# Kernel optimization log

Hardware: AMD Instinct MI355X
Metric: run time of the kernel (lower is better)

The kernel has to match this reference:

```python
import jax, jax.numpy as jnp
import numpy as np

N, E, K = 50000, 800000, 16
D, H = 128, 8
DH = D // H
SCALE = D ** (-0.5)
EPS = 1e-5


def _ln(x, g, b):
    m = jnp.mean(x, axis=-1, keepdims=True)
    v = jnp.mean((x - m) ** 2, axis=-1, keepdims=True)
    return (x - m) * jax.lax.rsqrt(v + EPS) * g + b


def setup_inputs() -> dict:
    key = jax.random.key(0)
    ks = jax.random.split(key, 20)
    s = 0.02
    inp = {
        "triplet_h": jax.random.normal(ks[0], (N, D), jnp.float32),
        "mask_nodes": jnp.ones((N,), jnp.bool_),
        "src": jax.random.randint(ks[1], (E,), 0, N),
        "dst": jax.random.randint(ks[2], (E,), 0, N),
        "edge_bias": jax.random.normal(ks[3], (E, H), jnp.float32),
        "mask_edges": jnp.ones((E,), jnp.bool_),
        "inc_idx": jax.random.randint(ks[4], (N, K), 0, E),
        "inc_mask": jnp.ones((N, K), jnp.bool_),
        # params
        "ln1_g": jnp.ones((D,), jnp.float32),
        "ln1_b": jnp.zeros((D,), jnp.float32),
        "qkv_w": jax.random.normal(ks[5], (D, 3 * D), jnp.float32) * s,
        "qkv_b": jnp.zeros((3 * D,), jnp.float32),
        "res_in_w": jax.random.normal(ks[6], (D, D), jnp.float32) * s,
        "res_in_b": jnp.zeros((D,), jnp.float32),
        "res_ln_g": jnp.ones((D,), jnp.float32),
        "res_ln_b": jnp.zeros((D,), jnp.float32),
        "ffn_in_w": jax.random.normal(ks[7], (D, 4 * D), jnp.float32) * s,
        "ffn_in_b": jnp.zeros((4 * D,), jnp.float32),
        "ffn_out_w": jax.random.normal(ks[8], (4 * D, D), jnp.float32) * s,
        "ffn_out_b": jnp.zeros((D,), jnp.float32),
    }
    return inp


def reference(triplet_h, mask_nodes, src, dst, edge_bias, mask_edges, inc_idx,
              inc_mask, ln1_g, ln1_b, qkv_w, qkv_b, res_in_w, res_in_b,
              res_ln_g, res_ln_b, ffn_in_w, ffn_in_b, ffn_out_w, ffn_out_b):
    x = _ln(triplet_h, ln1_g, ln1_b)
    qkv = (x @ qkv_w + qkv_b).reshape(-1, 3, H, DH)
    q = qkv[:, 0] * SCALE  # [N,H,dh]
    k = qkv[:, 1]
    v = qkv[:, 2]

    zero_i = jnp.zeros_like(src)
    se = jnp.where(mask_edges, src, zero_i)
    de = jnp.where(mask_edges, dst, zero_i)

    dot_all = jnp.sum(q[se] * k[de], axis=-1)  # [E,H]
    me = mask_edges[:, None]
    dot_all = jnp.where(me, dot_all, 0.0)
    eb = jnp.where(me, edge_bias, 0.0)
    scores_all = dot_all + eb  # [E,H]

    v_src = jnp.where(me[:, :, None], v[se], 0.0)  # [E,H,dh]

    idx = jnp.clip(inc_idx, 0)  # [N,K]
    s_in = scores_all[idx]  # [N,K,H]
    v_in = v_src[idx]       # [N,K,H,dh]
    m_in = inc_mask & mask_nodes[:, None]
    s_in = jnp.where(m_in[:, :, None], s_in, -1e9)
    a_in = jax.nn.softmax(s_in, axis=1)  # [N,K,H]
    out = jnp.sum(v_in * a_in[..., None], axis=1).reshape(-1, H * DH)  # [N,D]

    # Residual block (dropout p=0)
    x2 = triplet_h + (out @ res_in_w + res_in_b)
    y = _ln(x2, res_ln_g, res_ln_b)
    y = jax.nn.gelu(y @ ffn_in_w + ffn_in_b) @ ffn_out_w + ffn_out_b
    return x2 + y
```

## Files before the change

### kernel.cpp

```cpp
#include <hip/hip_runtime.h>
#include <math.h>

#define N_NODES 50000
#define N_EDGES 800000
#define QSCALE 0.08838834764831845f
#define LEPS 1e-5f
#define S4 0.17f
#define INV_S4 (1.0f / S4)
#define SC4 (S4 * S4 * QSCALE)

typedef unsigned short ushort_t;
typedef unsigned char uchar_t;
typedef short bf16x8 __attribute__((ext_vector_type(8)));
typedef float f32x4 __attribute__((ext_vector_type(4)));
typedef float f32x2 __attribute__((ext_vector_type(2)));

__device__ __forceinline__ ushort_t f2b(float f) {
    unsigned int u = __float_as_uint(f);
    u += 0x7FFF + ((u >> 16) & 1);
    return (ushort_t)(u >> 16);
}
__device__ __forceinline__ float b2f(ushort_t v) {
    return __uint_as_float(((unsigned int)v) << 16);
}
__device__ __forceinline__ uchar_t f2fp8(float f) {
    unsigned int pk = __builtin_amdgcn_cvt_pk_fp8_f32(f, f, 0, false);
    return (uchar_t)(pk & 0xff);
}
__device__ __forceinline__ float gelu_f(float x) {
    float u = 1.5957691216057308f * (x + 0.044715f * x * x * x);
    float e = __expf(u);
    float t = 1.f - 2.f / (e + 1.f);
    return 0.5f * x * (1.f + t);
}
__device__ __forceinline__ void gload16(const ushort_t* g, ushort_t* l) {
    __builtin_amdgcn_global_load_lds(
        (const __attribute__((address_space(1))) unsigned int*)g,
        (__attribute__((address_space(3))) unsigned int*)l, 16, 0, 0);
}
__device__ __forceinline__ int frag_idx(int n7, int k7) {
    return ((n7 >> 4) * 4 + (k7 >> 5)) * 512 + ((k7 >> 3) & 3) * 128 + (n7 & 15) * 8 + (k7 & 7);
}
__device__ __forceinline__ int fidx64(int n7, int k6) {
    return ((n7 >> 4) * 2 + (k6 >> 5)) * 512 + ((k6 >> 3) & 3) * 128 + (n7 & 15) * 8 + (k6 & 7);
}

#if __has_builtin(__builtin_amdgcn_sdot8)
__device__ __forceinline__ int snib_dot(unsigned int a, unsigned int b, int acc) {
    return __builtin_amdgcn_sdot8((int)a, (int)b, acc, false);
}
#else
__device__ __forceinline__ int snib_dot(unsigned int a, unsigned int b, int acc) {
    #pragma unroll
    for (int i = 0; i < 8; ++i) {
        int av = (int)((a >> (4 * i)) & 15u); av = (av ^ 8) - 8;
        int bv = (int)((b >> (4 * i)) & 15u); bv = (bv ^ 8) - 8;
        acc += av * bv;
    }
    return acc;
}
#endif

__global__ __launch_bounds__(256) void k_prep(
    const float* __restrict__ qkvw, const float* __restrict__ riw,
    const float* __restrict__ fiw,  const float* __restrict__ fow,
    const int* __restrict__ src, const int* __restrict__ dst,
    const float* __restrict__ eb,
    ushort_t* __restrict__ qkvwT, ushort_t* __restrict__ riwT,
    ushort_t* __restrict__ fiwT,  ushort_t* __restrict__ fowT,
    uint4* __restrict__ edt)
{
    if (blockIdx.x >= 768) {
        int i = (blockIdx.x - 768) * 256 + threadIdx.x;
        if (i >= N_EDGES) return;
        float4 a = *(const float4*)(eb + (size_t)i * 8);
        float4 b = *(const float4*)(eb + (size_t)i * 8 + 4);
        uint4 r0, r1;
        r0.x = (unsigned int)src[i];
        r0.y = (unsigned int)dst[i];
        r0.z = (unsigned int)f2b(a.x) | ((unsigned int)f2b(a.y) << 16);
        r0.w = (unsigned int)f2b(a.z) | ((unsigned int)f2b(a.w) << 16);
        r1.x = (unsigned int)f2b(b.x) | ((unsigned int)f2b(b.y) << 16);
        r1.y = (unsigned int)f2b(b.z) | ((unsigned int)f2b(b.w) << 16);
        r1.z = 0; r1.w = 0;
        edt[(size_t)i * 2]     = r0;
        edt[(size_t)i * 2 + 1] = r1;
        return;
    }
    int i = blockIdx.x * 256 + threadIdx.x;
    if (i < 384 * 128) {
        int k = i / 384, n = i - k * 384;
        int ch = n >> 7, n7 = n & 127, half = k >> 6, k6 = k & 63;
        qkvwT[(size_t)(ch * 2 + half) * 8192 + fidx64(n7, k6)] = f2b(qkvw[i]);
        return;
    }
    i -= 384 * 128;
    if (i < 128 * 128) {
        int k = i >> 7, n = i & 127;
        riwT[frag_idx(n, k)] = f2b(riw[i]);
        return;
    }
    i -= 128 * 128;
    if (i < 512 * 128) {
        int k = i >> 9, n = i & 511;
        fiwT[(size_t)(n >> 7) * 16384 + frag_idx(n & 127, k)] = f2b(fiw[i]);
        return;
    }
    i -= 512 * 128;
    if (i < 128 * 512) {
        int k = i >> 7, n = i & 127;
        fowT[(size_t)(k >> 6) * 8192 + fidx64(n, k & 63)] = f2b(fow[i]);
    }
}

__global__ __launch_bounds__(256) void k1_ln_qkv(
    const float* __restrict__ th, const float* __restrict__ g1, const float* __restrict__ b1,
    const ushort_t* __restrict__ wT, const float* __restrict__ bias,
    uchar_t* __restrict__ q4, uchar_t* __restrict__ k4, uchar_t* __restrict__ v8)
{
    __shared__ __align__(16) ushort_t xs[64][136];
    __shared__ __align__(16) ushort_t wbuf[2][8192];
    const int tid = threadIdx.x, lane = tid & 63, w = tid >> 6;
    const int g0 = blockIdx.x * 64;
    uchar_t* sbuf8 = (uchar_t*)xs;

    #pragma unroll
    for (int t = 0; t < 4; ++t)
        gload16(wT + (size_t)(t * 256 + tid) * 8, wbuf[0] + (t * 256 + tid) * 8);

    float ga = g1[lane], gb = g1[lane + 64];
    float ba = b1[lane], bb = b1[lane + 64];
    for (int rr = 0; rr < 16; ++rr) {
        int r = w * 16 + rr, grow = g0 + r;
        float x0 = 0.f, x1 = 0.f;
        if (grow < N_NODES) {
            x0 = th[(size_t)grow * 128 + lane];
            x1 = th[(size_t)grow * 128 + 64 + lane];
        }
        float s1 = x0 + x1, s2 = x0 * x0 + x1 * x1;
        #pragma unroll
        for (int off = 32; off; off >>= 1) { s1 += __shfl_xor(s1, off); s2 += __shfl_xor(s2, off); }
        float m = s1 * (1.f / 128.f);
        float v = s2 * (1.f / 128.f) - m * m;
        float rs = rsqrtf(v + LEPS);
        xs[r][lane]      = f2b((x0 - m) * rs * ga + ba);
        xs[r][lane + 64] = f2b((x1 - m) * rs * gb + bb);
    }
    __syncthreads();

    const int q = lane >> 4, ml = lane & 15;
    const int rloc = w * 16 + q * 4;
    bf16x8 a[4];
    #pragma unroll
    for (int kc = 0; kc < 4; ++kc)
        a[kc] = *(const bf16x8*)&xs[w * 16 + ml][kc * 32 + q * 8];

    for (int ch = 0; ch < 3; ++ch) {
        f32x4 acc[8];
        #pragma unroll
        for (int t2 = 0; t2 < 8; ++t2) acc[t2] = (f32x4){0.f, 0.f, 0.f, 0.f};

        #pragma unroll
        for (int t = 0; t < 4; ++t)
            gload16(wT + (size_t)(ch * 2 + 1) * 8192 + (size_t)(t * 256 + tid) * 8,
                    wbuf[1] + (t * 256 + tid) * 8);
        {
            const bf16x8* wb8 = (const bf16x8*)wbuf[0];
            #pragma unroll
            for (int t2 = 0; t2 < 8; ++t2)
                #pragma unroll
                for (int kc2 = 0; kc2 < 2; ++kc2)
                    acc[t2] = __builtin_amdgcn_mfma_f32_16x16x32_bf16(
                        a[kc2], wb8[(t2 * 2 + kc2) * 64 + lane], acc[t2], 0, 0, 0);
        }
        __syncthreads();

        if (ch < 2) {
            #pragma unroll
            for (int t = 0; t < 4; ++t)
                gload16(wT + (size_t)(ch + 1) * 2 * 8192 + (size_t)(t * 256 + tid) * 8,
                        wbuf[0] + (t * 256 + tid) * 8);
        }
        {
            const bf16x8* wb8 = (const bf16x8*)wbuf[1];
            #pragma unroll
            for (int t2 = 0; t2 < 8; ++t2)
                #pragma unroll
                for (int kc2 = 0; kc2 < 2; ++kc2)
                    acc[t2] = __builtin_amdgcn_mfma_f32_16x16x32_bf16(
                        a[2 + kc2], wb8[(t2 * 2 + kc2) * 64 + lane], acc[t2], 0, 0, 0);
        }
        __syncthreads();

        #pragma unroll
        for (int t2 = 0; t2 < 8; ++t2) {
            int n = t2 * 16 + ml;
            float bs = bias[ch * 128 + n];
            #pragma unroll
            for (int r = 0; r < 4; ++r) {
                float val = acc[t2][r] + bs;
                if (ch < 2) {
                    float enc = rintf(val * INV_S4) + 8.f;
                    enc = fminf(fmaxf(enc, 0.f), 15.f);
                    sbuf8[(rloc + r) * 128 + n] = ((uchar_t)enc) ^ 8;
                } else {
                    sbuf8[(rloc + r) * 128 + n] = f2fp8(val);
                }
            }
        }
        __syncthreads();
        if (ch < 2) {
            uchar_t* outp = (ch == 0) ? q4 : k4;
            int grow = g0 + (tid >> 2);
            if (grow < N_NODES) {
                const uchar_t* in = sbuf8 + (tid >> 2) * 128 + (tid & 3) * 32;
                uint4 o;
                unsigned int* ow = (unsigned int*)&o;
                #pragma unroll
                for (int wd = 0; wd < 4; ++wd) {
                    unsigned int x = 0;
                    #pragma unroll
                    for (int b = 0; b < 4; ++b) {
                        unsigned int lo = in[wd * 8 + 2 * b];
                        unsigned int hi = in[wd * 8 + 2 * b + 1];
                        x |= (lo | (hi << 4)) << (8 * b);
                    }
                    ow[wd] = x;
                }
                *(uint4*)(outp + (size_t)grow * 64 + (tid & 3) * 16) = o;
            }
        } else {
            int grow = g0 + (tid >> 2);
            if (grow < N_NODES) {
                uint4 v0 = *(const uint4*)(sbuf8 + tid * 32);
                uint4 v1 = *(const uint4*)(sbuf8 + tid * 32 + 16);
                *(uint4*)(v8 + (size_t)grow * 128 + (tid & 3) * 32) = v0;
                *(uint4*)(v8 + (size_t)grow * 128 + (tid & 3) * 32 + 16) = v1;
            }
        }
    }
}

__global__ __launch_bounds__(256) void k23_agg(
    const uchar_t* __restrict__ q4, const uchar_t* __restrict__ k4,
    const uchar_t* __restrict__ v8,
    const uint4* __restrict__ edt,
    const int* __restrict__ inc_idx,
    ushort_t* __restrict__ outw)
{
    __shared__ int ss[256];
    __shared__ float sc[16 * 144];
    const int tid = threadIdx.x;
    const int nb = blockIdx.x * 16;

    {
        int e = inc_idx[(size_t)nb * 16 + tid];
        if (e < 0) e = 0;
        uint4 r0 = edt[(size_t)e * 2];
        uint4 r1 = edt[(size_t)e * 2 + 1];
        int s = (int)r0.x, d = (int)r0.y;
        ss[tid] = s;
        const uint4 qa = *(const uint4*)(q4 + (size_t)s * 64);
        const uint4 qb = *(const uint4*)(q4 + (size_t)s * 64 + 16);
        const uint4 qc = *(const uint4*)(q4 + (size_t)s * 64 + 32);
        const uint4 qd = *(const uint4*)(q4 + (size_t)s * 64 + 48);
        const uint4 ka = *(const uint4*)(k4 + (size_t)d * 64);
        const uint4 kb = *(const uint4*)(k4 + (size_t)d * 64 + 16);
        const uint4 kc = *(const uint4*)(k4 + (size_t)d * 64 + 32);
        const uint4 kd = *(const uint4*)(k4 + (size_t)d * 64 + 48);
        int d0 = snib_dot(qa.x, ka.x, snib_dot(qa.y, ka.y, 0));
        int d1 = snib_dot(qa.z, ka.z, snib_dot(qa.w, ka.w, 0));
        int d2 = snib_dot(qb.x, kb.x, snib_dot(qb.y, kb.y, 0));
        int d3 = snib_dot(qb.z, kb.z, snib_dot(qb.w, kb.w, 0));
        int d4 = snib_dot(qc.x, kc.x, snib_dot(qc.y, kc.y, 0));
        int d5 = snib_dot(qc.z, kc.z, snib_dot(qc.w, kc.w, 0));
        int d6 = snib_dot(qd.x, kd.x, snib_dot(qd.y, kd.y, 0));
        int d7 = snib_dot(qd.z, kd.z, snib_dot(qd.w, kd.w, 0));
        float* scn = sc + (tid >> 4) * 144 + (tid & 15) * 9;
        scn[0] = (float)d0 * SC4 + b2f((ushort_t)(r0.z & 0xffff));
        scn[1] = (float)d1 * SC4 + b2f((ushort_t)(r0.z >> 16));
        scn[2] = (float)d2 * SC4 + b2f((ushort_t)(r0.w & 0xffff));
        scn[3] = (float)d3 * SC4 + b2f((ushort_t)(r0.w >> 16));
        scn[4] = (float)d4 * SC4 + b2f((ushort_t)(r1.x & 0xffff));
        scn[5] = (float)d5 * SC4 + b2f((ushort_t)(r1.x >> 16));
        scn[6] = (float)d6 * SC4 + b2f((ushort_t)(r1.y & 0xffff));
        scn[7] = (float)d7 * SC4 + b2f((ushort_t)(r1.y >> 16));
    }
    __syncthreads();

    const int node = tid >> 4;
    const int lx = tid & 15;
    const int h = lx >> 1;
    const int j0 = lx * 8;
    const float* scn = sc + node * 144 + h;
    float m = -1e30f;
    #pragma unroll
    for (int k = 0; k < 16; k++) m = fmaxf(m, scn[k * 9]);
    float p[16];
    float sum = 0.f;
    #pragma unroll
    for (int k = 0; k < 16; k++) { p[k] = __expf(scn[k * 9] - m); sum += p[k]; }
    float inv = 1.f / sum;
    f32x2 A0 = {0.f, 0.f}, A1 = {0.f, 0.f}, A2 = {0.f, 0.f}, A3 = {0.f, 0.f};
    #pragma unroll
    for (int k = 0; k < 16; k++) {
        int sn = ss[node * 16 + k];
        uint2 vv = *(const uint2*)(v8 + (size_t)sn * 128 + j0);
        f32x2 u0 = __builtin_amdgcn_cvt_pk_f32_fp8(vv.x, false);
        f32x2 u1 = __builtin_amdgcn_cvt_pk_f32_fp8(vv.x, true);
        f32x2 u2 = __builtin_amdgcn_cvt_pk_f32_fp8(vv.y, false);
        f32x2 u3 = __builtin_amdgcn_cvt_pk_f32_fp8(vv.y, true);
        f32x2 pk2 = {p[k], p[k]};
        A0 += u0 * pk2; A1 += u1 * pk2; A2 += u2 * pk2; A3 += u3 * pk2;
    }
    uint4 o;
    o.x = (unsigned int)f2b(A0.x * inv) | ((unsigned int)f2b(A0.y * inv) << 16);
    o.y = (unsigned int)f2b(A1.x * inv) | ((unsigned int)f2b(A1.y * inv) << 16);
    o.z = (unsigned int)f2b(A2.x * inv) | ((unsigned int)f2b(A2.y * inv) << 16);
    o.w = (unsigned int)f2b(A3.x * inv) | ((unsigned int)f2b(A3.y * inv) << 16);
    *(uint4*)(outw + (size_t)(nb + node) * 128 + j0) = o;
}

__global__ __launch_bounds__(256) void k4_ffn(
    const float* __restrict__ th, const ushort_t* __restrict__ outw,
    const ushort_t* __restrict__ riwT, const float* __restrict__ rib,
    const float* __restrict__ rlg, const float* __restrict__ rlb,
    const ushort_t* __restrict__ fiwT, const float* __restrict__ fib,
    const ushort_t* __restrict__ fowT, const float* __restrict__ fob,
    float* __restrict__ dout)
{
    __shared__ __align__(16) ushort_t sbuf[64][136];
    __shared__ __align__(16) ushort_t wbuf[2][8192];
    const int tid = threadIdx.x, lane = tid & 63, w = tid >> 6;
    const int g0 = blockIdx.x * 64;
    const int q = lane >> 4, ml = lane & 15;
    const int rloc = w * 16 + q * 4;
    const int aswz = (ml >> 2) & 3;
    const bf16x8* wb0 = (const bf16x8*)wbuf[0];
    const bf16x8* wb1 = (const bf16x8*)wbuf[1];

    #pragma unroll
    for (int t = 0; t < 4; ++t)
        gload16(riwT + (size_t)(t * 256 + tid) * 8, wbuf[0] + (t * 256 + tid) * 8);
    int arow = g0 + w * 16 + ml; if (arow > N_NODES - 1) arow = N_NODES - 1;
    bf16x8 a[4];
    #pragma unroll
    for (int kc = 0; kc < 4; ++kc)
        a[kc] = *(const bf16x8*)(outw + (size_t)arow * 128 + kc * 32 + q * 8);
    float tv[8][4];
    #pragma unroll
    for (int t = 0; t < 8; ++t)
        #pragma unroll
        for (int r = 0; r < 4; ++r) {
            int grow = g0 + rloc + r;
            tv[t][r] = (grow < N_NODES) ? th[(size_t)grow * 128 + t * 16 + ml] : 0.f;
        }
    __syncthreads();

    f32x4 acc[8];

    #pragma unroll
    for (int t = 0; t < 4; ++t)
        gload16(riwT + 8192 + (size_t)(t * 256 + tid) * 8, wbuf[1] + (t * 256 + tid) * 8);
    #pragma unroll
    for (int t2 = 0; t2 < 4; ++t2) {
        f32x4 z = {0.f, 0.f, 0.f, 0.f};
        #pragma unroll
        for (int kc = 0; kc < 4; ++kc)
            z = __builtin_amdgcn_mfma_f32_16x16x32_bf16(
                a[kc], wb0[(t2 * 4 + kc) * 64 + lane], z, 0, 0, 0);
        acc[t2] = z;
    }
    __syncthreads();

    #pragma unroll
    for (int t = 0; t < 4; ++t)
        gload16(fiwT + (size_t)(t * 256 + tid) * 8, wbuf[0] + (t * 256 + tid) * 8);
    #pragma unroll
    for (int t2 = 0; t2 < 4; ++t2) {
        f32x4 z = {0.f, 0.f, 0.f, 0.f};
        #pragma unroll
        for (int kc = 0; kc < 4; ++kc)
            z = __builtin_amdgcn_mfma_f32_16x16x32_bf16(
                a[kc], wb1[(t2 * 4 + kc) * 64 + lane], z, 0, 0, 0);
        acc[4 + t2] = z;
    }
    #pragma unroll
    for (int t = 0; t < 8; ++t) {
        float bb = rib[t * 16 + ml];
        #pragma unroll
        for (int r = 0; r < 4; ++r)
            acc[t][r] += bb + tv[t][r];
    }
    {
        float rg[8], rbv[8];
        #pragma unroll
        for (int t = 0; t < 8; ++t) { rg[t] = rlg[t * 16 + ml]; rbv[t] = rlb[t * 16 + ml]; }
        #pragma unroll
        for (int r = 0; r < 4; ++r) {
            float s1 = 0.f, s2 = 0.f;
            #pragma unroll
            for (int t = 0; t < 8; ++t) { float v = acc[t][r]; s1 += v; s2 += v * v; }
            #pragma unroll
            for (int off = 1; off < 16; off <<= 1) { s1 += __shfl_xor(s1, off); s2 += __shfl_xor(s2, off); }
            float m = s1 * (1.f / 128.f);
            float v = s2 * (1.f / 128.f) - m * m;
            float rs = rsqrtf(v + LEPS);
            #pragma unroll
            for (int t = 0; t < 8; ++t) {
                int G = (2 * t + (ml >> 3)) ^ q;
                sbuf[rloc + r][G * 8 + (ml & 7)] = f2b((acc[t][r] - m) * rs * rg[t] + rbv[t]);
            }
        }
    }
    bf16x8 a2[4];
    #pragma unroll
    for (int kc = 0; kc < 4; ++kc)
        a2[kc] = *(const bf16x8*)&sbuf[w * 16 + ml][(((kc * 4 + q) ^ aswz) << 3)];
    __syncthreads();

    for (int f = 0; f < 8; ++f) {
        #pragma unroll
        for (int t = 0; t < 4; ++t)
            gload16(fowT + (size_t)f * 8192 + (size_t)(t * 256 + tid) * 8,
                    wbuf[1] + (t * 256 + tid) * 8);
        #pragma unroll
        for (int t2 = 0; t2 < 4; ++t2) {
            f32x4 hacc = {0.f, 0.f, 0.f, 0.f};
            #pragma unroll
            for (int kc = 0; kc < 4; ++kc)
                hacc = __builtin_amdgcn_mfma_f32_16x16x32_bf16(
                    a2[kc], wb0[(t2 * 4 + kc) * 64 + lane], hacc, 0, 0, 0);
            float fb = fib[f * 64 + t2 * 16 + ml];
            int G = (2 * t2 + (ml >> 3)) ^ q;
            #pragma unroll
            for (int r = 0; r < 4; ++r)
                sbuf[rloc + r][G * 8 + (ml & 7)] = f2b(gelu_f(hacc[r] + fb));
        }
        bf16x8 a3[2];
        #pragma unroll
        for (int kc2 = 0; kc2 < 2; ++kc2)
            a3[kc2] = *(const bf16x8*)&sbuf[w * 16 + ml][(((kc2 * 4 + q) ^ aswz) << 3)];
        __syncthreads();

        if (f < 7) {
            #pragma unroll
            for (int t = 0; t < 4; ++t)
                gload16(fiwT + (size_t)(f + 1) * 8192 + (size_t)(t * 256 + tid) * 8,
                        wbuf[0] + (t * 256 + tid) * 8);
        }
        #pragma unroll
        for (int t = 0; t < 8; ++t) {
            #pragma unroll
            for (int kc2 = 0; kc2 < 2; ++kc2)
                acc[t] = __builtin_amdgcn_mfma_f32_16x16x32_bf16(
                    a3[kc2], wb1[(t * 2 + kc2) * 64 + lane], acc[t], 0, 0, 0);
        }
        __syncthreads();
    }

    #pragma unroll
    for (int t = 0; t < 8; ++t) {
        float ob = fob[t * 16 + ml];
        #pragma unroll
        for (int r = 0; r < 4; ++r) {
            int grow = g0 + rloc + r;
            if (grow < N_NODES)
                dout[(size_t)grow * 128 + t * 16 + ml] = acc[t][r] + ob;
        }
    }
}

extern "C" void kernel_launch(void* const* d_in, const int* in_sizes, int n_in,
                              void* d_out, int out_size, void* d_ws, size_t ws_size,
                              hipStream_t stream)
{
    const float* th    = (const float*)d_in[0];
    const int*   src   = (const int*)d_in[2];
    const int*   dst   = (const int*)d_in[3];
    const float* ebias = (const float*)d_in[4];
    const int*   inc   = (const int*)d_in[6];
    const float* ln1g  = (const float*)d_in[8];
    const float* ln1b  = (const float*)d_in[9];
    const float* qkvw  = (const float*)d_in[10];
    const float* qkvb  = (const float*)d_in[11];
    const float* riw   = (const float*)d_in[12];
    const float* rib   = (const float*)d_in[13];
    const float* rlg   = (const float*)d_in[14];
    const float* rlb   = (const float*)d_in[15];
    const float* fiw   = (const float*)d_in[16];
    const float* fib   = (const float*)d_in[17];
    const float* fow   = (const float*)d_in[18];
    const float* fob   = (const float*)d_in[19];

    char* ws = (char*)d_ws;
    uchar_t* q4      = (uchar_t*)ws;                               ws += (size_t)N_NODES * 64;
    uchar_t* k4t     = (uchar_t*)ws;                               ws += (size_t)N_NODES * 64;
    uchar_t* v8      = (uchar_t*)ws;                               ws += (size_t)N_NODES * 128;
    ushort_t* outw   = (ushort_t*)ws;                              ws += (size_t)N_NODES * 128 * 2;
    ushort_t* qkvwT  = (ushort_t*)ws;                              ws += (size_t)384 * 128 * 2;
    ushort_t* riwT   = (ushort_t*)ws;                              ws += (size_t)128 * 128 * 2;
    ushort_t* fiwT   = (ushort_t*)ws;                              ws += (size_t)512 * 128 * 2;
    ushort_t* fowT   = (ushort_t*)ws;                              ws += (size_t)128 * 512 * 2;
    uint4*    edt    = (uint4*)ws;                                 ws += (size_t)N_EDGES * 32;
    float* dout = (float*)d_out;

    k_prep<<<768 + (N_EDGES + 255) / 256, 256, 0, stream>>>(
        qkvw, riw, fiw, fow, src, dst, ebias, qkvwT, riwT, fiwT, fowT, edt);
    k1_ln_qkv<<<(N_NODES + 63) / 64, 256, 0, stream>>>(th, ln1g, ln1b, qkvwT, qkvb, q4, k4t, v8);
    k23_agg<<<N_NODES / 16, 256, 0, stream>>>(q4, k4t, v8, edt, inc, outw);
    k4_ffn<<<(N_NODES + 63) / 64, 256, 0, stream>>>(th, outw, riwT, rib, rlg, rlb,
                                                    fiwT, fib, fowT, fob, dout);
}
```

Measured before the change: 275.1 us.

## Split FFN kernel output columns across wave pairs with 512-thread blocks

The fused residual/LN/FFN kernel now runs 512 threads per block: each 16-row group is handled by two waves, each owning half of the 128 output columns. LayerNorm statistics are combined across the wave pair through a small shared-memory reduction. Biases and gamma/beta are preloaded into registers, and the weight-tile loads are rescheduled. The aim is to halve per-wave accumulator registers and MFMA work so more waves are resident and latency is better hidden. The cost is extra __syncthreads and more barrier stalls per FFN chunk.

```diff
diff --git a/kernel.cpp b/kernel.cpp
--- a/kernel.cpp
+++ b/kernel.cpp
@@ -321,7 +321,7 @@
     *(uint4*)(outw + (size_t)(nb + node) * 128 + j0) = o;
 }
 
-__global__ __launch_bounds__(256) void k4_ffn(
+__global__ __launch_bounds__(512, 4) void k4_ffn(
     const float* __restrict__ th, const ushort_t* __restrict__ outw,
     const ushort_t* __restrict__ riwT, const float* __restrict__ rib,
     const float* __restrict__ rlg, const float* __restrict__ rlb,
@@ -331,142 +331,150 @@
 {
     __shared__ __align__(16) ushort_t sbuf[64][136];
     __shared__ __align__(16) ushort_t wbuf[2][8192];
+    __shared__ float lnred[4][16][2][2];
     const int tid = threadIdx.x, lane = tid & 63, w = tid >> 6;
+    const int p = w >> 1, hn = w & 1;
     const int g0 = blockIdx.x * 64;
     const int q = lane >> 4, ml = lane & 15;
-    const int rloc = w * 16 + q * 4;
+    const int rloc = p * 16 + q * 4;
     const int aswz = (ml >> 2) & 3;
     const bf16x8* wb0 = (const bf16x8*)wbuf[0];
     const bf16x8* wb1 = (const bf16x8*)wbuf[1];
 
     #pragma unroll
-    for (int t = 0; t < 4; ++t)
-        gload16(riwT + (size_t)(t * 256 + tid) * 8, wbuf[0] + (t * 256 + tid) * 8);
-    int arow = g0 + w * 16 + ml; if (arow > N_NODES - 1) arow = N_NODES - 1;
+    for (int t = 0; t < 2; ++t)
+        gload16(riwT + (size_t)(t * 512 + tid) * 8, wbuf[0] + (t * 512 + tid) * 8);
+    #pragma unroll
+    for (int t = 0; t < 2; ++t)
+        gload16(riwT + 8192 + (size_t)(t * 512 + tid) * 8, wbuf[1] + (t * 512 + tid) * 8);
+
+    int arow = g0 + p * 16 + ml; if (arow > N_NODES - 1) arow = N_NODES - 1;
     bf16x8 a[4];
     #pragma unroll
     for (int kc = 0; kc < 4; ++kc)
         a[kc] = *(const bf16x8*)(outw + (size_t)arow * 128 + kc * 32 + q * 8);
-    float tv[8][4];
-    #pragma unroll
-    for (int t = 0; t < 8; ++t)
+    float tv[4][4];
+    #pragma unroll
+    for (int t = 0; t < 4; ++t)
         #pragma unroll
         for (int r = 0; r < 4; ++r) {
             int grow = g0 + rloc + r;
-            tv[t][r] = (grow < N_NODES) ? th[(size_t)grow * 128 + t * 16 + ml] : 0.f;
-        }
-    __syncthreads();
-
-    f32x4 acc[8];
-
-    #pragma unroll
-    for (int t = 0; t < 4; ++t)
-        gload16(riwT + 8192 + (size_t)(t * 256 + tid) * 8, wbuf[1] + (t * 256 + tid) * 8);
-    #pragma unroll
-    for (int t2 = 0; t2 < 4; ++t2) {
+            tv[t][r] = (grow < N_NODES) ? th[(size_t)grow * 128 + hn * 64 + t * 16 + ml] : 0.f;
+        }
+    float fibr[16];
+    #pragma unroll
+    for (int f = 0; f < 8; ++f)
+        #pragma unroll
+        for (int t2 = 0; t2 < 2; ++t2)
+            fibr[f * 2 + t2] = fib[f * 64 + (hn * 2 + t2) * 16 + ml];
+    float rbias[4], rg[4], rbv[4], fb4[4];
+    #pragma unroll
+    for (int t = 0; t < 4; ++t) {
+        int c = hn * 64 + t * 16 + ml;
+        rbias[t] = rib[c]; rg[t] = rlg[c]; rbv[t] = rlb[c]; fb4[t] = fob[c];
+    }
+    __syncthreads();
+
+    const bf16x8* wbg = hn ? wb1 : wb0;
+    f32x4 acc[4];
+    #pragma unroll
+    for (int t = 0; t < 4; ++t) {
         f32x4 z = {0.f, 0.f, 0.f, 0.f};
         #pragma unroll
         for (int kc = 0; kc < 4; ++kc)
             z = __builtin_amdgcn_mfma_f32_16x16x32_bf16(
-                a[kc], wb0[(t2 * 4 + kc) * 64 + lane], z, 0, 0, 0);
-        acc[t2] = z;
-    }
-    __syncthreads();
-
-    #pragma unroll
-    for (int t = 0; t < 4; ++t)
-        gload16(fiwT + (size_t)(t * 256 + tid) * 8, wbuf[0] + (t * 256 + tid) * 8);
-    #pragma unroll
-    for (int t2 = 0; t2 < 4; ++t2) {
-        f32x4 z = {0.f, 0.f, 0.f, 0.f};
-        #pragma unroll
-        for (int kc = 0; kc < 4; ++kc)
-            z = __builtin_amdgcn_mfma_f32_16x16x32_bf16(
-                a[kc], wb1[(t2 * 4 + kc) * 64 + lane], z, 0, 0, 0);
-        acc[4 + t2] = z;
-    }
-    #pragma unroll
-    for (int t = 0; t < 8; ++t) {
-        float bb = rib[t * 16 + ml];
-        #pragma unroll
-        for (int r = 0; r < 4; ++r)
-            acc[t][r] += bb + tv[t][r];
-    }
-    {
-        float rg[8], rbv[8];
-        #pragma unroll
-        for (int t = 0; t < 8; ++t) { rg[t] = rlg[t * 16 + ml]; rbv[t] = rlb[t * 16 + ml]; }
-        #pragma unroll
-        for (int r = 0; r < 4; ++r) {
-            float s1 = 0.f, s2 = 0.f;
-            #pragma unroll
-            for (int t = 0; t < 8; ++t) { float v = acc[t][r]; s1 += v; s2 += v * v; }
-            #pragma unroll
-            for (int off = 1; off < 16; off <<= 1) { s1 += __shfl_xor(s1, off); s2 += __shfl_xor(s2, off); }
-            float m = s1 * (1.f / 128.f);
-            float v = s2 * (1.f / 128.f) - m * m;
-            float rs = rsqrtf(v + LEPS);
-            #pragma unroll
-            for (int t = 0; t < 8; ++t) {
-                int G = (2 * t + (ml >> 3)) ^ q;
-                sbuf[rloc + r][G * 8 + (ml & 7)] = f2b((acc[t][r] - m) * rs * rg[t] + rbv[t]);
-            }
-        }
-    }
+                a[kc], wbg[(t * 4 + kc) * 64 + lane], z, 0, 0, 0);
+        #pragma unroll
+        for (int r = 0; r < 4; ++r) z[r] += rbias[t] + tv[t][r];
+        acc[t] = z;
+    }
+    float ps1[4], ps2[4];
+    #pragma unroll
+    for (int r = 0; r < 4; ++r) {
+        float s1 = 0.f, s2 = 0.f;
+        #pragma unroll
+        for (int t = 0; t < 4; ++t) { float v = acc[t][r]; s1 += v; s2 += v * v; }
+        #pragma unroll
+        for (int off = 1; off < 16; off <<= 1) { s1 += __shfl_xor(s1, off); s2 += __shfl_xor(s2, off); }
+        ps1[r] = s1; ps2[r] = s2;
+        if (ml == 0) { lnred[p][q * 4 + r][hn][0] = s1; lnred[p][q * 4 + r][hn][1] = s2; }
+    }
+    __syncthreads();
+    #pragma unroll
+    for (int r = 0; r < 4; ++r) {
+        float s1 = ps1[r] + lnred[p][q * 4 + r][hn ^ 1][0];
+        float s2 = ps2[r] + lnred[p][q * 4 + r][hn ^ 1][1];
+        float m = s1 * (1.f / 128.f);
+        float v = s2 * (1.f / 128.f) - m * m;
+        float rs = rsqrtf(v + LEPS);
+        #pragma unroll
+        for (int t = 0; t < 4; ++t) {
+            int G = (2 * (hn * 4 + t) + (ml >> 3)) ^ q;
+            sbuf[rloc + r][G * 8 + (ml & 7)] = f2b((acc[t][r] - m) * rs * rg[t] + rbv[t]);
+        }
+    }
+    __syncthreads();
     bf16x8 a2[4];
     #pragma unroll
     for (int kc = 0; kc < 4; ++kc)
-        a2[kc] = *(const bf16x8*)&sbuf[w * 16 + ml][(((kc * 4 + q) ^ aswz) << 3)];
+        a2[kc] = *(const bf16x8*)&sbuf[p * 16 + ml][(((kc * 4 + q) ^ aswz) << 3)];
+    __syncthreads();
+    #pragma unroll
+    for (int t = 0; t < 2; ++t)
+        gload16(fiwT + (size_t)(t * 512 + tid) * 8, wbuf[0] + (t * 512 + tid) * 8);
+    #pragma unroll
+    for (int t = 0; t < 2; ++t)
+        gload16(fowT + (size_t)(t * 512 + tid) * 8, wbuf[1] + (t * 512 + tid) * 8);
     __syncthreads();
 
     for (int f = 0; f < 8; ++f) {
         #pragma unroll
-        for (int t = 0; t < 4; ++t)
-            gload16(fowT + (size_t)f * 8192 + (size_t)(t * 256 + tid) * 8,
-                    wbuf[1] + (t * 256 + tid) * 8);
-        #pragma unroll
-        for (int t2 = 0; t2 < 4; ++t2) {
+        for (int t2 = 0; t2 < 2; ++t2) {
             f32x4 hacc = {0.f, 0.f, 0.f, 0.f};
             #pragma unroll
             for (int kc = 0; kc < 4; ++kc)
                 hacc = __builtin_amdgcn_mfma_f32_16x16x32_bf16(
-                    a2[kc], wb0[(t2 * 4 + kc) * 64 + lane], hacc, 0, 0, 0);
-            float fb = fib[f * 64 + t2 * 16 + ml];
-            int G = (2 * t2 + (ml >> 3)) ^ q;
+                    a2[kc], wb0[((hn * 2 + t2) * 4 + kc) * 64 + lane], hacc, 0, 0, 0);
+            float fb = fibr[f * 2 + t2];
+            int G = (2 * (hn * 2 + t2) + (ml >> 3)) ^ q;
             #pragma unroll
             for (int r = 0; r < 4; ++r)
                 sbuf[rloc + r][G * 8 + (ml & 7)] = f2b(gelu_f(hacc[r] + fb));
         }
+        __syncthreads();
+        if (f < 7) {
+            #pragma unroll
+            for (int t = 0; t < 2; ++t)
+                gload16(fiwT + (size_t)(f + 1) * 8192 + (size_t)(t * 512 + tid) * 8,
+                        wbuf[0] + (t * 512 + tid) * 8);
+        }
         bf16x8 a3[2];
         #pragma unroll
         for (int kc2 = 0; kc2 < 2; ++kc2)
-            a3[kc2] = *(const bf16x8*)&sbuf[w * 16 + ml][(((kc2 * 4 + q) ^ aswz) << 3)];
-        __syncthreads();
-
-        if (f < 7) {
-            #pragma unroll
-            for (int t = 0; t < 4; ++t)
-                gload16(fiwT + (size_t)(f + 1) * 8192 + (size_t)(t * 256 + tid) * 8,
-                        wbuf[0] + (t * 256 + tid) * 8);
-        }
-        #pragma unroll
-        for (int t = 0; t < 8; ++t) {
+            a3[kc2] = *(const bf16x8*)&sbuf[p * 16 + ml][(((kc2 * 4 + q) ^ aswz) << 3)];
+        #pragma unroll
+        for (int t = 0; t < 4; ++t) {
             #pragma unroll
             for (int kc2 = 0; kc2 < 2; ++kc2)
                 acc[t] = __builtin_amdgcn_mfma_f32_16x16x32_bf16(
-                    a3[kc2], wb1[(t * 2 + kc2) * 64 + lane], acc[t], 0, 0, 0);
+                    a3[kc2], wb1[((hn * 4 + t) * 2 + kc2) * 64 + lane], acc[t], 0, 0, 0);
         }
         __syncthreads();
-    }
-
-    #pragma unroll
-    for (int t = 0; t < 8; ++t) {
-        float ob = fob[t * 16 + ml];
+        if (f < 7) {
+            #pragma unroll
+            for (int t = 0; t < 2; ++t)
+                gload16(fowT + (size_t)(f + 1) * 8192 + (size_t)(t * 512 + tid) * 8,
+                        wbuf[1] + (t * 512 + tid) * 8);
+        }
+    }
+
+    #pragma unroll
+    for (int t = 0; t < 4; ++t) {
         #pragma unroll
         for (int r = 0; r < 4; ++r) {
             int grow = g0 + rloc + r;
             if (grow < N_NODES)
-                dout[(size_t)grow * 128 + t * 16 + ml] = acc[t][r] + ob;
+                dout[(size_t)grow * 128 + hn * 64 + t * 16 + ml] = acc[t][r] + fb4[t];
         }
     }
 }
@@ -509,6 +517,6 @@
         qkvw, riw, fiw, fow, src, dst, ebias, qkvwT, riwT, fiwT, fowT, edt);
     k1_ln_qkv<<<(N_NODES + 63) / 64, 256, 0, stream>>>(th, ln1g, ln1b, qkvwT, qkvb, q4, k4t, v8);
     k23_agg<<<N_NODES / 16, 256, 0, stream>>>(q4, k4t, v8, edt, inc, outw);
-    k4_ffn<<<(N_NODES + 63) / 64, 256, 0, stream>>>(th, outw, riwT, rib, rlg, rlb,
+    k4_ffn<<<(N_NODES + 63) / 64, 512, 0, stream>>>(th, outw, riwT, rib, rlg, rlb,
                                                     fiwT, fib, fowT, fob, dout);
 }
```

Result: no change. 270.3 us (-1.7%).

## Double FFN kernel row tile to 128 rows per block to reuse staged weights

Applied to the files above, without the earlier changes.

The fused residual/FFN kernel now processes 128 node rows per 256-thread block, with each wave handling two 16-row MMA tiles. Every weight chunk staged in shared memory is therefore used for twice as many rows, which halves global weight traffic and the per-row cost of barriers. The residual input load moves after the first GEMM to ease register pressure, and a minimum of two blocks per CU is requested. The trade-off is twice the accumulator registers, a larger shared buffer, and half as many blocks, which can lower occupancy or cause spills.

```diff
diff --git a/kernel.cpp b/kernel.cpp
--- a/kernel.cpp
+++ b/kernel.cpp
@@ -321,7 +321,7 @@
     *(uint4*)(outw + (size_t)(nb + node) * 128 + j0) = o;
 }
 
-__global__ __launch_bounds__(256) void k4_ffn(
+__global__ __launch_bounds__(256, 2) void k4_ffn(
     const float* __restrict__ th, const ushort_t* __restrict__ outw,
     const ushort_t* __restrict__ riwT, const float* __restrict__ rib,
     const float* __restrict__ rlg, const float* __restrict__ rlb,
@@ -329,12 +329,11 @@
     const ushort_t* __restrict__ fowT, const float* __restrict__ fob,
     float* __restrict__ dout)
 {
-    __shared__ __align__(16) ushort_t sbuf[64][136];
+    __shared__ __align__(16) ushort_t sbuf[128][136];
     __shared__ __align__(16) ushort_t wbuf[2][8192];
     const int tid = threadIdx.x, lane = tid & 63, w = tid >> 6;
-    const int g0 = blockIdx.x * 64;
+    const int g0 = blockIdx.x * 128;
     const int q = lane >> 4, ml = lane & 15;
-    const int rloc = w * 16 + q * 4;
     const int aswz = (ml >> 2) & 3;
     const bf16x8* wb0 = (const bf16x8*)wbuf[0];
     const bf16x8* wb1 = (const bf16x8*)wbuf[1];
@@ -342,81 +341,94 @@
     #pragma unroll
     for (int t = 0; t < 4; ++t)
         gload16(riwT + (size_t)(t * 256 + tid) * 8, wbuf[0] + (t * 256 + tid) * 8);
-    int arow = g0 + w * 16 + ml; if (arow > N_NODES - 1) arow = N_NODES - 1;
-    bf16x8 a[4];
-    #pragma unroll
-    for (int kc = 0; kc < 4; ++kc)
-        a[kc] = *(const bf16x8*)(outw + (size_t)arow * 128 + kc * 32 + q * 8);
-    float tv[8][4];
-    #pragma unroll
-    for (int t = 0; t < 8; ++t)
-        #pragma unroll
-        for (int r = 0; r < 4; ++r) {
-            int grow = g0 + rloc + r;
-            tv[t][r] = (grow < N_NODES) ? th[(size_t)grow * 128 + t * 16 + ml] : 0.f;
-        }
+    bf16x8 a[2][4];
+    #pragma unroll
+    for (int m2 = 0; m2 < 2; ++m2) {
+        int arow = g0 + w * 32 + m2 * 16 + ml;
+        if (arow > N_NODES - 1) arow = N_NODES - 1;
+        #pragma unroll
+        for (int kc = 0; kc < 4; ++kc)
+            a[m2][kc] = *(const bf16x8*)(outw + (size_t)arow * 128 + kc * 32 + q * 8);
+    }
     __syncthreads();
 
-    f32x4 acc[8];
+    f32x4 acc[2][8];
 
     #pragma unroll
     for (int t = 0; t < 4; ++t)
         gload16(riwT + 8192 + (size_t)(t * 256 + tid) * 8, wbuf[1] + (t * 256 + tid) * 8);
     #pragma unroll
-    for (int t2 = 0; t2 < 4; ++t2) {
-        f32x4 z = {0.f, 0.f, 0.f, 0.f};
-        #pragma unroll
-        for (int kc = 0; kc < 4; ++kc)
-            z = __builtin_amdgcn_mfma_f32_16x16x32_bf16(
-                a[kc], wb0[(t2 * 4 + kc) * 64 + lane], z, 0, 0, 0);
-        acc[t2] = z;
-    }
+    for (int m2 = 0; m2 < 2; ++m2)
+        #pragma unroll
+        for (int t2 = 0; t2 < 4; ++t2) {
+            f32x4 z = {0.f, 0.f, 0.f, 0.f};
+            #pragma unroll
+            for (int kc = 0; kc < 4; ++kc)
+                z = __builtin_amdgcn_mfma_f32_16x16x32_bf16(
+                    a[m2][kc], wb0[(t2 * 4 + kc) * 64 + lane], z, 0, 0, 0);
+            acc[m2][t2] = z;
+        }
     __syncthreads();
 
     #pragma unroll
     for (int t = 0; t < 4; ++t)
         gload16(fiwT + (size_t)(t * 256 + tid) * 8, wbuf[0] + (t * 256 + tid) * 8);
     #pragma unroll
-    for (int t2 = 0; t2 < 4; ++t2) {
-        f32x4 z = {0.f, 0.f, 0.f, 0.f};
-        #pragma unroll
-        for (int kc = 0; kc < 4; ++kc)
-            z = __builtin_amdgcn_mfma_f32_16x16x32_bf16(
-                a[kc], wb1[(t2 * 4 + kc) * 64 + lane], z, 0, 0, 0);
-        acc[4 + t2] = z;
-    }
-    #pragma unroll
-    for (int t = 0; t < 8; ++t) {
-        float bb = rib[t * 16 + ml];
-        #pragma unroll
-        for (int r = 0; r < 4; ++r)
-            acc[t][r] += bb + tv[t][r];
+    for (int m2 = 0; m2 < 2; ++m2)
+        #pragma unroll
+        for (int t2 = 0; t2 < 4; ++t2) {
+            f32x4 z = {0.f, 0.f, 0.f, 0.f};
+            #pragma unroll
+            for (int kc = 0; kc < 4; ++kc)
+                z = __builtin_amdgcn_mfma_f32_16x16x32_bf16(
+                    a[m2][kc], wb1[(t2 * 4 + kc) * 64 + lane], z, 0, 0, 0);
+            acc[m2][4 + t2] = z;
+        }
+    #pragma unroll
+    for (int m2 = 0; m2 < 2; ++m2) {
+        const int rloc = w * 32 + m2 * 16 + q * 4;
+        #pragma unroll
+        for (int t = 0; t < 8; ++t) {
+            float bb = rib[t * 16 + ml];
+            #pragma unroll
+            for (int r = 0; r < 4; ++r) {
+                int grow = g0 + rloc + r;
+                float tv = (grow < N_NODES) ? th[(size_t)grow * 128 + t * 16 + ml] : 0.f;
+                acc[m2][t][r] += bb + tv;
+            }
+        }
     }
     {
         float rg[8], rbv[8];
         #pragma unroll
         for (int t = 0; t < 8; ++t) { rg[t] = rlg[t * 16 + ml]; rbv[t] = rlb[t * 16 + ml]; }
         #pragma unroll
-        for (int r = 0; r < 4; ++r) {
-            float s1 = 0.f, s2 = 0.f;
-            #pragma unroll
-            for (int t = 0; t < 8; ++t) { float v = acc[t][r]; s1 += v; s2 += v * v; }
-            #pragma unroll
-            for (int off = 1; off < 16; off <<= 1) { s1 += __shfl_xor(s1, off); s2 += __shfl_xor(s2, off); }
-            float m = s1 * (1.f / 128.f);
-            float v = s2 * (1.f / 128.f) - m * m;
-            float rs = rsqrtf(v + LEPS);
-            #pragma unroll
-            for (int t = 0; t < 8; ++t) {
-                int G = (2 * t + (ml >> 3)) ^ q;
-                sbuf[rloc + r][G * 8 + (ml & 7)] = f2b((acc[t][r] - m) * rs * rg[t] + rbv[t]);
-            }
-        }
-    }
-    bf16x8 a2[4];
-    #pragma unroll
-    for (int kc = 0; kc < 4; ++kc)
-        a2[kc] = *(const bf16x8*)&sbuf[w * 16 + ml][(((kc * 4 + q) ^ aswz) << 3)];
+        for (int m2 = 0; m2 < 2; ++m2) {
+            const int rloc = w * 32 + m2 * 16 + q * 4;
+            #pragma unroll
+            for (int r = 0; r < 4; ++r) {
+                float s1 = 0.f, s2 = 0.f;
+                #pragma unroll
+                for (int t = 0; t < 8; ++t) { float v = acc[m2][t][r]; s1 += v; s2 += v * v; }
+                #pragma unroll
+                for (int off = 1; off < 16; off <<= 1) { s1 += __shfl_xor(s1, off); s2 += __shfl_xor(s2, off); }
+                float m = s1 * (1.f / 128.f);
+                float v = s2 * (1.f / 128.f) - m * m;
+                float rs = rsqrtf(v + LEPS);
+                #pragma unroll
+                for (int t = 0; t < 8; ++t) {
+                    int G = (2 * t + (ml >> 3)) ^ q;
+                    sbuf[rloc + r][G * 8 + (ml & 7)] = f2b((acc[m2][t][r] - m) * rs * rg[t] + rbv[t]);
+                }
+            }
+        }
+    }
+    bf16x8 a2[2][4];
+    #pragma unroll
+    for (int m2 = 0; m2 < 2; ++m2)
+        #pragma unroll
+        for (int kc = 0; kc < 4; ++kc)
+            a2[m2][kc] = *(const bf16x8*)&sbuf[w * 32 + m2 * 16 + ml][(((kc * 4 + q) ^ aswz) << 3)];
     __syncthreads();
 
     for (int f = 0; f < 8; ++f) {
@@ -425,22 +437,28 @@
             gload16(fowT + (size_t)f * 8192 + (size_t)(t * 256 + tid) * 8,
                     wbuf[1] + (t * 256 + tid) * 8);
         #pragma unroll
-        for (int t2 = 0; t2 < 4; ++t2) {
-            f32x4 hacc = {0.f, 0.f, 0.f, 0.f};
-            #pragma unroll
-            for (int kc = 0; kc < 4; ++kc)
-                hacc = __builtin_amdgcn_mfma_f32_16x16x32_bf16(
-                    a2[kc], wb0[(t2 * 4 + kc) * 64 + lane], hacc, 0, 0, 0);
-            float fb = fib[f * 64 + t2 * 16 + ml];
-            int G = (2 * t2 + (ml >> 3)) ^ q;
-            #pragma unroll
-            for (int r = 0; r < 4; ++r)
-                sbuf[rloc + r][G * 8 + (ml & 7)] = f2b(gelu_f(hacc[r] + fb));
-        }
-        bf16x8 a3[2];
-        #pragma unroll
-        for (int kc2 = 0; kc2 < 2; ++kc2)
-            a3[kc2] = *(const bf16x8*)&sbuf[w * 16 + ml][(((kc2 * 4 + q) ^ aswz) << 3)];
+        for (int m2 = 0; m2 < 2; ++m2) {
+            const int rloc = w * 32 + m2 * 16 + q * 4;
+            #pragma unroll
+            for (int t2 = 0; t2 < 4; ++t2) {
+                f32x4 hacc = {0.f, 0.f, 0.f, 0.f};
+                #pragma unroll
+                for (int kc = 0; kc < 4; ++kc)
+                    hacc = __builtin_amdgcn_mfma_f32_16x16x32_bf16(
+                        a2[m2][kc], wb0[(t2 * 4 + kc) * 64 + lane], hacc, 0, 0, 0);
+                float fb = fib[f * 64 + t2 * 16 + ml];
+                int G = (2 * t2 + (ml >> 3)) ^ q;
+                #pragma unroll
+                for (int r = 0; r < 4; ++r)
+                    sbuf[rloc + r][G * 8 + (ml & 7)] = f2b(gelu_f(hacc[r] + fb));
+            }
+        }
+        bf16x8 a3[2][2];
+        #pragma unroll
+        for (int m2 = 0; m2 < 2; ++m2)
+            #pragma unroll
+            for (int kc2 = 0; kc2 < 2; ++kc2)
+                a3[m2][kc2] = *(const bf16x8*)&sbuf[w * 32 + m2 * 16 + ml][(((kc2 * 4 + q) ^ aswz) << 3)];
         __syncthreads();
 
         if (f < 7) {
@@ -450,23 +468,29 @@
                         wbuf[0] + (t * 256 + tid) * 8);
         }
         #pragma unroll
+        for (int m2 = 0; m2 < 2; ++m2)
+            #pragma unroll
+            for (int t = 0; t < 8; ++t) {
+                #pragma unroll
+                for (int kc2 = 0; kc2 < 2; ++kc2)
+                    acc[m2][t] = __builtin_amdgcn_mfma_f32_16x16x32_bf16(
+                        a3[m2][kc2], wb1[(t * 2 + kc2) * 64 + lane], acc[m2][t], 0, 0, 0);
+            }
+        __syncthreads();
+    }
+
+    #pragma unroll
+    for (int m2 = 0; m2 < 2; ++m2) {
+        const int rloc = w * 32 + m2 * 16 + q * 4;
+        #pragma unroll
         for (int t = 0; t < 8; ++t) {
-            #pragma unroll
-            for (int kc2 = 0; kc2 < 2; ++kc2)
-                acc[t] = __builtin_amdgcn_mfma_f32_16x16x32_bf16(
-                    a3[kc2], wb1[(t * 2 + kc2) * 64 + lane], acc[t], 0, 0, 0);
-        }
-        __syncthreads();
-    }
-
-    #pragma unroll
-    for (int t = 0; t < 8; ++t) {
-        float ob = fob[t * 16 + ml];
-        #pragma unroll
-        for (int r = 0; r < 4; ++r) {
-            int grow = g0 + rloc + r;
-            if (grow < N_NODES)
-                dout[(size_t)grow * 128 + t * 16 + ml] = acc[t][r] + ob;
+            float ob = fob[t * 16 + ml];
+            #pragma unroll
+            for (int r = 0; r < 4; ++r) {
+                int grow = g0 + rloc + r;
+                if (grow < N_NODES)
+                    dout[(size_t)grow * 128 + t * 16 + ml] = acc[m2][t][r] + ob;
+            }
         }
     }
 }
@@ -509,6 +533,6 @@
         qkvw, riw, fiw, fow, src, dst, ebias, qkvwT, riwT, fiwT, fowT, edt);
     k1_ln_qkv<<<(N_NODES + 63) / 64, 256, 0, stream>>>(th, ln1g, ln1b, qkvwT, qkvb, q4, k4t, v8);
     k23_agg<<<N_NODES / 16, 256, 0, stream>>>(q4, k4t, v8, edt, inc, outw);
-    k4_ffn<<<(N_NODES + 63) / 64, 256, 0, stream>>>(th, outw, riwT, rib, rlg, rlb,
-                                                    fiwT, fib, fowT, fob, dout);
-}
+    k4_ffn<<<(N_NODES + 127) / 128, 256, 0, stream>>>(th, outw, riwT, rib, rlg, rlb,
+                                                      fiwT, fib, fowT, fob, dout);
+}
```

After: 273.0 us. No clear change (-0.7%).
